# Performance work log

Measured on AMD Instinct MI355X. Metric: run time of the kernel, lower is better.

Reference implementation:

```python
import jax, jax.numpy as jnp
import numpy as np

D = 256   # input / vocab dim (hardcoded in module)
H = 256   # hidden_dim
B, M, N = 64, 32, 32
LN_EPS = 1e-6


def setup_inputs() -> dict:
    key = jax.random.key(0)
    ks = jax.random.split(key, 8)
    Hin = D + 2 * H  # column_stack([x_bd, h_i_jm1, h_im1_j])
    inp = {
        "x": jax.random.normal(ks[0], (B, M, N, D), dtype=jnp.float32),
        "W_gate": jax.random.normal(ks[1], (Hin, 5 * H), dtype=jnp.float32) * (1.0 / np.sqrt(Hin)),
        "b_gate": jnp.zeros((5 * H,), dtype=jnp.float32),
        "ln_scale": jnp.ones((H,), dtype=jnp.float32),
        "ln_bias": jnp.zeros((H,), dtype=jnp.float32),
        "W_head": jax.random.normal(ks[2], (H, D), dtype=jnp.float32) * (1.0 / np.sqrt(H)),
        "b_head": jnp.zeros((D,), dtype=jnp.float32),
        "h_init": jax.random.normal(ks[3], (H, 1), dtype=jnp.float32) * 0.05,
    }
    return inp


def _layernorm(x, scale, bias):
    mu = jnp.mean(x, axis=-1, keepdims=True)
    var = jnp.mean(jnp.square(x - mu), axis=-1, keepdims=True)
    return (x - mu) * jax.lax.rsqrt(var + LN_EPS) * scale + bias


def reference(x, W_gate, b_gate, ln_scale, ln_bias, W_head, b_head, h_init):
    b, m, n, d = x.shape
    h = h_init.shape[0]
    h0_bh = jnp.broadcast_to(h_init[:, 0][None, :], (b, h))  # left-edge init per row
    c0_bh = jnp.zeros((b, h), dtype=x.dtype)

    def col_step(carry, xs):
        h_l, c_l = carry                 # left neighbor (b,h)
        x_bd, h_u, c_u = xs              # input pixel, up-neighbor h/c
        xin = jnp.concatenate([x_bd, h_l, h_u], axis=-1)   # (b, d+2h)
        g = xin @ W_gate + b_gate                           # (b, 5h)
        f_c, f_r, i_g, o_g, g_g = jnp.split(g, 5, axis=-1)
        cell = (jax.nn.sigmoid(f_c) * c_l
                + jax.nn.sigmoid(f_r) * c_u
                + jax.nn.sigmoid(i_g) * jnp.tanh(g_g))      # (b,h)
        h_new = jax.nn.sigmoid(o_g) * jnp.tanh(_layernorm(cell, ln_scale, ln_bias))
        logits = h_new @ W_head + b_head                    # (b,d)
        return (h_new, cell), (h_new, cell, logits)

    def row_step(prev_row, x_row):
        prev_h, prev_c = prev_row        # (n,b,h) from row above
        _, (hs, cs, logits) = jax.lax.scan(col_step, (h0_bh, c0_bh), (x_row, prev_h, prev_c))
        return (hs, cs), logits          # logits: (n,b,d)

    x_mnbd = jnp.transpose(x, (1, 2, 0, 3))                 # (m,n,b,d)
    prev_h0 = jnp.broadcast_to(h_init[:, 0][None, None, :], (n, b, h)).astype(x.dtype)
    prev_c0 = jnp.zeros((n, b, h), dtype=x.dtype)
    _, logits_mnbd = jax.lax.scan(row_step, (prev_h0, prev_c0), x_mnbd)
    return jnp.transpose(logits_mnbd, (2, 0, 1, 3))         # (b,m,n,d)
```

## Files before the change

### kernel.cpp

```cpp
#include <hip/hip_runtime.h>

constexpr int kB   = 64;
constexpr int kM   = 32;
constexpr int kN   = 32;
constexpr int kD   = 256;
constexpr int kH   = 256;
constexpr int kG5  = 1280;

typedef __attribute__((ext_vector_type(8)))  short bf16x8;
typedef __attribute__((ext_vector_type(16))) float f32x16;

__device__ __forceinline__ float bu2f(unsigned short u) {
    return __uint_as_float(((unsigned)u) << 16);
}
__device__ __forceinline__ unsigned short f2bu(float f) {
    unsigned u = __float_as_uint(f);
    return (unsigned short)((u + 0x7FFF + ((u >> 16) & 1)) >> 16);
}
__device__ __forceinline__ void split1(float a, unsigned short& hi, unsigned short& lo) {
    hi = f2bu(a);
    lo = f2bu(a - bu2f(hi));
}
__device__ __forceinline__ float sigm(float x) { return 1.f / (1.f + expf(-x)); }

__global__ void prep_w(const float* __restrict__ Wg,
                       unsigned short* __restrict__ whi,
                       unsigned short* __restrict__ wlo) {
    const int t = blockIdx.x * 256 + threadIdx.x;
    const int lane = t & 63;
    const int rest = t >> 6;
    const int s = rest % 48;
    const int ntile = rest / 48;
    const int n = ntile * 32 + (lane & 31);
    const int kb = s * 16 + (lane >> 5) * 8;
    unsigned short h8[8], l8[8];
    #pragma unroll
    for (int j = 0; j < 8; ++j) {
        const float a = Wg[(size_t)(kb + j) * kG5 + n];
        split1(a, h8[j], l8[j]);
    }
    *(bf16x8*)(whi + (size_t)t * 8) = *(const bf16x8*)h8;
    *(bf16x8*)(wlo + (size_t)t * 8) = *(const bf16x8*)l8;
}

__global__ void prep_wh(const float* __restrict__ Wh,
                        unsigned short* __restrict__ whh,
                        unsigned short* __restrict__ whl) {
    const int t = blockIdx.x * 256 + threadIdx.x;
    const int lane = t & 63;
    const int rest = t >> 6;
    const int kc = rest & 15;
    const int nt = rest >> 4;
    const int n = nt * 32 + (lane & 31);
    const int kb = kc * 16 + (lane >> 5) * 8;
    unsigned short h8[8], l8[8];
    #pragma unroll
    for (int j = 0; j < 8; ++j) {
        const float a = Wh[(size_t)(kb + j) * kD + n];
        split1(a, h8[j], l8[j]);
    }
    *(bf16x8*)(whh + (size_t)t * 8) = *(const bf16x8*)h8;
    *(bf16x8*)(whl + (size_t)t * 8) = *(const bf16x8*)l8;
}

__global__ void prep_h0f(const float* __restrict__ hinit,
                         unsigned short* __restrict__ h0fh,
                         unsigned short* __restrict__ h0fl) {
    const int idx = blockIdx.x * 256 + threadIdx.x;
    const int lane = idx & 63;
    const int kh = idx >> 6;
    const int k0 = kh * 16 + (lane >> 5) * 8;
    unsigned short h8[8], l8[8];
    #pragma unroll
    for (int j = 0; j < 8; ++j) split1(hinit[k0 + j], h8[j], l8[j]);
    *(bf16x8*)(h0fh + (size_t)idx * 8) = *(const bf16x8*)h8;
    *(bf16x8*)(h0fl + (size_t)idx * 8) = *(const bf16x8*)l8;
}

__global__ void prep_x(const float* __restrict__ x,
                       unsigned short* __restrict__ xfh,
                       unsigned short* __restrict__ xfl) {
    const int t = blockIdx.x * 256 + threadIdx.x;
    const int kq   = t & 31;
    const int b    = (t >> 5) & 63;
    const int cell = t >> 11;
    const float* src = x + (((size_t)b * 1024 + cell) * kD + kq * 8);
    unsigned short h8[8], l8[8];
    #pragma unroll
    for (int j = 0; j < 8; ++j) split1(src[j], h8[j], l8[j]);
    const int mt = b >> 5, kh = kq >> 1;
    const int l  = (b & 31) + 32 * (kq & 1);
    const size_t dst = ((((size_t)cell * 2 + mt) * 16 + kh) * 64 + l) * 8;
    *(bf16x8*)(xfh + dst) = *(const bf16x8*)h8;
    *(bf16x8*)(xfl + dst) = *(const bf16x8*)l8;
}

template<bool SYNCW>
__device__ __forceinline__
void gate_body(int d, int unit,
               const unsigned short* __restrict__ xfh,
               const unsigned short* __restrict__ xfl,
               const unsigned short* __restrict__ whi,
               const unsigned short* __restrict__ wlo,
               const unsigned short* __restrict__ hfh,
               const unsigned short* __restrict__ hfl,
               const unsigned short* __restrict__ h0fh,
               const unsigned short* __restrict__ h0fl,
               float* __restrict__ gates) {
    const int tid = threadIdx.x;
    const int ilo = max(0, d - (kN - 1));
    const int cell = unit / 20;
    const int nc   = unit % 20;
    const int i = ilo + cell;
    const int j = d - i;
    const int w = tid >> 6, lane = tid & 63;
    const int ln31 = lane & 31, ln5 = lane >> 5;
    const int mt = w & 1;
    const int ntile = nc * 2 + (w >> 1);
    const int hp = (d + 1) & 1;
    const int cl = i * kN + j;

    f32x16 acc;
    #pragma unroll
    for (int r = 0; r < 16; ++r) acc[r] = 0.f;

    const unsigned short* wph = whi + ((size_t)ntile * 3072 + lane) * 8;
    const unsigned short* wpl = wlo + ((size_t)ntile * 3072 + lane) * 8;

    const unsigned short* xph = xfh + (((size_t)cl * 2 + mt) * 16 * 64 + lane) * 8;
    const unsigned short* xpl = xfl + (((size_t)cl * 2 + mt) * 16 * 64 + lane) * 8;
    #pragma unroll
    for (int kw = 0; kw < 4; ++kw) {
        if (SYNCW) __syncthreads();
        #pragma unroll
        for (int k4 = 0; k4 < 4; ++k4) {
            const int kh = kw * 4 + k4;
            const bf16x8 ah = *(const bf16x8*)(xph + (size_t)kh * 512);
            const bf16x8 al = *(const bf16x8*)(xpl + (size_t)kh * 512);
            const bf16x8 wh = *(const bf16x8*)(wph + (size_t)kh * 512);
            const bf16x8 wl = *(const bf16x8*)(wpl + (size_t)kh * 512);
            acc = __builtin_amdgcn_mfma_f32_32x32x16_bf16(ah, wh, acc, 0, 0, 0);
            acc = __builtin_amdgcn_mfma_f32_32x32x16_bf16(ah, wl, acc, 0, 0, 0);
            acc = __builtin_amdgcn_mfma_f32_32x32x16_bf16(al, wh, acc, 0, 0, 0);
        }
    }

    const unsigned short *plh, *pll, *puh, *pul;
    if (j > 0) {
        const size_t o = ((size_t)(hp * kM + i)) * 16384 + ((size_t)(mt * 16) * 64 + lane) * 8;
        plh = hfh + o; pll = hfl + o;
    } else {
        plh = h0fh + lane * 8; pll = h0fl + lane * 8;
    }
    if (i > 0) {
        const size_t o = ((size_t)(hp * kM + (i - 1))) * 16384 + ((size_t)(mt * 16) * 64 + lane) * 8;
        puh = hfh + o; pul = hfl + o;
    } else {
        puh = h0fh + lane * 8; pul = h0fl + lane * 8;
    }

    #pragma unroll
    for (int kw = 0; kw < 4; ++kw) {
        if (SYNCW) __syncthreads();
        #pragma unroll
        for (int k4 = 0; k4 < 4; ++k4) {
            const int kh = kw * 4 + k4;
            const bf16x8 ah = *(const bf16x8*)(plh + (size_t)kh * 512);
            const bf16x8 al = *(const bf16x8*)(pll + (size_t)kh * 512);
            const bf16x8 wh = *(const bf16x8*)(wph + (size_t)(16 + kh) * 512);
            const bf16x8 wl = *(const bf16x8*)(wpl + (size_t)(16 + kh) * 512);
            acc = __builtin_amdgcn_mfma_f32_32x32x16_bf16(ah, wh, acc, 0, 0, 0);
            acc = __builtin_amdgcn_mfma_f32_32x32x16_bf16(ah, wl, acc, 0, 0, 0);
            acc = __builtin_amdgcn_mfma_f32_32x32x16_bf16(al, wh, acc, 0, 0, 0);
        }
    }
    #pragma unroll
    for (int kw = 0; kw < 4; ++kw) {
        if (SYNCW) __syncthreads();
        #pragma unroll
        for (int k4 = 0; k4 < 4; ++k4) {
            const int kh = kw * 4 + k4;
            const bf16x8 ah = *(const bf16x8*)(puh + (size_t)kh * 512);
            const bf16x8 al = *(const bf16x8*)(pul + (size_t)kh * 512);
            const bf16x8 wh = *(const bf16x8*)(wph + (size_t)(32 + kh) * 512);
            const bf16x8 wl = *(const bf16x8*)(wpl + (size_t)(32 + kh) * 512);
            acc = __builtin_amdgcn_mfma_f32_32x32x16_bf16(ah, wh, acc, 0, 0, 0);
            acc = __builtin_amdgcn_mfma_f32_32x32x16_bf16(ah, wl, acc, 0, 0, 0);
            acc = __builtin_amdgcn_mfma_f32_32x32x16_bf16(al, wh, acc, 0, 0, 0);
        }
    }

    const int col = ntile * 32 + ln31;
    #pragma unroll
    for (int r = 0; r < 16; ++r) {
        const int mrow = (r & 3) + 8 * (r >> 2) + 4 * ln5;
        const int bb = mt * 32 + mrow;
        gates[((size_t)i * kB + bb) * kG5 + col] = acc[r];
    }
}

__global__ __launch_bounds__(256)
void gate_fast(int d,
               const unsigned short* __restrict__ xfh,
               const unsigned short* __restrict__ xfl,
               const unsigned short* __restrict__ whi,
               const unsigned short* __restrict__ wlo,
               const unsigned short* __restrict__ hfh,
               const unsigned short* __restrict__ hfl,
               const unsigned short* __restrict__ h0fh,
               const unsigned short* __restrict__ h0fl,
               float* __restrict__ gates) {
    gate_body<false>(d, blockIdx.x, xfh, xfl, whi, wlo, hfh, hfl, h0fh, h0fl, gates);
}

__global__ __launch_bounds__(256)
void gate_sync(int d,
               const unsigned short* __restrict__ xfh,
               const unsigned short* __restrict__ xfl,
               const unsigned short* __restrict__ whi,
               const unsigned short* __restrict__ wlo,
               const unsigned short* __restrict__ hfh,
               const unsigned short* __restrict__ hfl,
               const unsigned short* __restrict__ h0fh,
               const unsigned short* __restrict__ h0fl,
               float* __restrict__ gates) {
    gate_body<true>(d, blockIdx.x, xfh, xfl, whi, wlo, hfh, hfl, h0fh, h0fl, gates);
}

__global__ __launch_bounds__(256)
void gate_mfma_legacy(int d,
               const float* __restrict__ x,
               const unsigned short* __restrict__ whi,
               const unsigned short* __restrict__ wlo,
               const unsigned short* __restrict__ hfh,
               const unsigned short* __restrict__ hfl,
               const unsigned short* __restrict__ h0fh,
               const unsigned short* __restrict__ h0fl,
               float* __restrict__ gates) {
    const int tid = threadIdx.x;
    const int ilo = max(0, d - (kN - 1));
    const int cell = blockIdx.x / 20;
    const int nc   = blockIdx.x % 20;
    const int i = ilo + cell;
    const int j = d - i;
    const int w = tid >> 6, lane = tid & 63;
    const int ln31 = lane & 31, ln5 = lane >> 5;
    const int mt = w & 1;
    const int ntile = nc * 2 + (w >> 1);
    const int hp = (d + 1) & 1;

    f32x16 acc;
    #pragma unroll
    for (int r = 0; r < 16; ++r) acc[r] = 0.f;

    const unsigned short* wph = whi + ((size_t)ntile * 3072 + lane) * 8;
    const unsigned short* wpl = wlo + ((size_t)ntile * 3072 + lane) * 8;

    const int b = mt * 32 + ln31;
    const float* xr = x + (((size_t)b * kM + i) * kN + j) * kD + ln5 * 8;
    #pragma unroll 4
    for (int kh = 0; kh < 16; ++kh) {
        const float4 v0 = *(const float4*)(xr + kh * 16);
        const float4 v1 = *(const float4*)(xr + kh * 16 + 4);
        unsigned short h8[8], l8[8];
        split1(v0.x, h8[0], l8[0]); split1(v0.y, h8[1], l8[1]);
        split1(v0.z, h8[2], l8[2]); split1(v0.w, h8[3], l8[3]);
        split1(v1.x, h8[4], l8[4]); split1(v1.y, h8[5], l8[5]);
        split1(v1.z, h8[6], l8[6]); split1(v1.w, h8[7], l8[7]);
        const bf16x8 ah = *(const bf16x8*)h8;
        const bf16x8 al = *(const bf16x8*)l8;
        const bf16x8 wh = *(const bf16x8*)(wph + (size_t)kh * 512);
        const bf16x8 wl = *(const bf16x8*)(wpl + (size_t)kh * 512);
        acc = __builtin_amdgcn_mfma_f32_32x32x16_bf16(ah, wh, acc, 0, 0, 0);
        acc = __builtin_amdgcn_mfma_f32_32x32x16_bf16(ah, wl, acc, 0, 0, 0);
        acc = __builtin_amdgcn_mfma_f32_32x32x16_bf16(al, wh, acc, 0, 0, 0);
    }

    const unsigned short *plh, *pll, *puh, *pul;
    if (j > 0) {
        const size_t o = ((size_t)(hp * kM + i)) * 16384 + ((size_t)(mt * 16) * 64 + lane) * 8;
        plh = hfh + o; pll = hfl + o;
    } else {
        plh = h0fh + lane * 8; pll = h0fl + lane * 8;
    }
    if (i > 0) {
        const size_t o = ((size_t)(hp * kM + (i - 1))) * 16384 + ((size_t)(mt * 16) * 64 + lane) * 8;
        puh = hfh + o; pul = hfl + o;
    } else {
        puh = h0fh + lane * 8; pul = h0fl + lane * 8;
    }

    #pragma unroll 4
    for (int kh = 0; kh < 16; ++kh) {
        const bf16x8 ah = *(const bf16x8*)(plh + (size_t)kh * 512);
        const bf16x8 al = *(const bf16x8*)(pll + (size_t)kh * 512);
        const bf16x8 wh = *(const bf16x8*)(wph + (size_t)(16 + kh) * 512);
        const bf16x8 wl = *(const bf16x8*)(wpl + (size_t)(16 + kh) * 512);
        acc = __builtin_amdgcn_mfma_f32_32x32x16_bf16(ah, wh, acc, 0, 0, 0);
        acc = __builtin_amdgcn_mfma_f32_32x32x16_bf16(ah, wl, acc, 0, 0, 0);
        acc = __builtin_amdgcn_mfma_f32_32x32x16_bf16(al, wh, acc, 0, 0, 0);
    }
    #pragma unroll 4
    for (int kh = 0; kh < 16; ++kh) {
        const bf16x8 ah = *(const bf16x8*)(puh + (size_t)kh * 512);
        const bf16x8 al = *(const bf16x8*)(pul + (size_t)kh * 512);
        const bf16x8 wh = *(const bf16x8*)(wph + (size_t)(32 + kh) * 512);
        const bf16x8 wl = *(const bf16x8*)(wpl + (size_t)(32 + kh) * 512);
        acc = __builtin_amdgcn_mfma_f32_32x32x16_bf16(ah, wh, acc, 0, 0, 0);
        acc = __builtin_amdgcn_mfma_f32_32x32x16_bf16(ah, wl, acc, 0, 0, 0);
        acc = __builtin_amdgcn_mfma_f32_32x32x16_bf16(al, wh, acc, 0, 0, 0);
    }

    const int col = ntile * 32 + ln31;
    #pragma unroll
    for (int r = 0; r < 16; ++r) {
        const int mrow = (r & 3) + 8 * (r >> 2) + 4 * ln5;
        const int bb = mt * 32 + mrow;
        gates[((size_t)i * kB + bb) * kG5 + col] = acc[r];
    }
}

__global__ __launch_bounds__(256)
void cell_ln(int d,
             const float* __restrict__ bg,
             const float* __restrict__ lns,
             const float* __restrict__ lnb,
             const float* __restrict__ gates,
             float* __restrict__ c_bufs,
             unsigned short* __restrict__ hfh,
             unsigned short* __restrict__ hfl,
             float* out) {
    __shared__ float red[8];
    const int tid = threadIdx.x;
    const int ilo = max(0, d - (kN - 1));
    const int i = ilo + (blockIdx.x >> 4);
    const int j = d - i;
    const int b0 = (blockIdx.x & 15) * 4;
    const int plane = kM * kB * kH;
    const float* c_prev = c_bufs + ((d + 1) & 1) * plane;
    float*       c_cur  = c_bufs + (d & 1) * plane;
    const int hp = d & 1;
    unsigned* outp = (unsigned*)out;

    const int u = tid;
    const float bg0 = bg[u];
    const float bg1 = bg[kH + u];
    const float bg2 = bg[2 * kH + u];
    const float bg3 = bg[3 * kH + u];
    const float bg4 = bg[4 * kH + u];
    const float lnsc = lns[u];
    const float lnbi = lnb[u];
    const int lane = tid & 63, wid = tid >> 6;
    const int kh = u >> 4, r = u & 15, jj = r & 7;

    for (int bl = 0; bl < 4; ++bl) {
        const int b = b0 + bl;
        const float* grow = gates + ((size_t)i * kB + b) * kG5;
        const float fc = grow[u] + bg0;
        const float fr = grow[kH + u] + bg1;
        const float ig = grow[2 * kH + u] + bg2;
        const float og = grow[3 * kH + u] + bg3;
        const float gg = grow[4 * kH + u] + bg4;
        const float cl = (j > 0) ? c_prev[((size_t)i * kB + b) * kH + u] : 0.f;
        const float cu = (i > 0) ? c_prev[((size_t)(i - 1) * kB + b) * kH + u] : 0.f;

        const float cell_v = sigm(fc) * cl + sigm(fr) * cu + sigm(ig) * tanhf(gg);
        c_cur[((size_t)i * kB + b) * kH + u] = cell_v;

        float s = cell_v, s2 = cell_v * cell_v;
        #pragma unroll
        for (int off = 32; off; off >>= 1) {
            s  += __shfl_down(s,  off, 64);
            s2 += __shfl_down(s2, off, 64);
        }
        if (lane == 0) { red[wid] = s; red[4 + wid] = s2; }
        __syncthreads();
        const float sum = red[0] + red[1] + red[2] + red[3];
        const float sq  = red[4] + red[5] + red[6] + red[7];
        __syncthreads();

        const float mu   = sum * (1.f / kH);
        const float var  = sq * (1.f / kH) - mu * mu;
        const float rstd = rsqrtf(var + 1e-6f);
        const float hv   = sigm(og) * tanhf((cell_v - mu) * rstd * lnsc + lnbi);

        unsigned short hb, lb;
        split1(hv, hb, lb);
        const int mt2 = b >> 5;
        const int fl = (b & 31) + 32 * (r >> 3);
        const size_t fo = ((size_t)(hp * kM + i)) * 16384
                        + (((size_t)(mt2 * 16 + kh) * 64 + fl) * 8 + jj);
        hfh[fo] = hb; hfl[fo] = lb;
        outp[(((size_t)b * kM + i) * kN + j) * kD + u] = (unsigned)hb | ((unsigned)lb << 16);
    }
}

__global__ __launch_bounds__(256)
void head_mfma(const unsigned short* __restrict__ whh,
               const unsigned short* __restrict__ whl,
               const float* __restrict__ bh,
               float* out) {
    const int tid = threadIdx.x;
    const int lane = tid & 63, w = tid >> 6;
    const int ln31 = lane & 31, ln5 = lane >> 5;
    const int r0 = blockIdx.x * 64;
    const int mt = w & 1, ng = w >> 1;
    unsigned* outp = (unsigned*)out;

    f32x16 acc[4];
    #pragma unroll
    for (int t = 0; t < 4; ++t)
        #pragma unroll
        for (int r = 0; r < 16; ++r) acc[t][r] = 0.f;

    const int m = r0 + mt * 32 + ln31;
    const unsigned* arow = outp + (size_t)m * kD + ln5 * 8;

    #pragma unroll 2
    for (int kc = 0; kc < 16; ++kc) {
        const uint4 p0 = *(const uint4*)(arow + kc * 16);
        const uint4 p1 = *(const uint4*)(arow + kc * 16 + 4);
        unsigned short h8[8], l8[8];
        h8[0] = (unsigned short)(p0.x & 0xffffu); l8[0] = (unsigned short)(p0.x >> 16);
        h8[1] = (unsigned short)(p0.y & 0xffffu); l8[1] = (unsigned short)(p0.y >> 16);
        h8[2] = (unsigned short)(p0.z & 0xffffu); l8[2] = (unsigned short)(p0.z >> 16);
        h8[3] = (unsigned short)(p0.w & 0xffffu); l8[3] = (unsigned short)(p0.w >> 16);
        h8[4] = (unsigned short)(p1.x & 0xffffu); l8[4] = (unsigned short)(p1.x >> 16);
        h8[5] = (unsigned short)(p1.y & 0xffffu); l8[5] = (unsigned short)(p1.y >> 16);
        h8[6] = (unsigned short)(p1.z & 0xffffu); l8[6] = (unsigned short)(p1.z >> 16);
        h8[7] = (unsigned short)(p1.w & 0xffffu); l8[7] = (unsigned short)(p1.w >> 16);
        const bf16x8 ah = *(const bf16x8*)h8;
        const bf16x8 al = *(const bf16x8*)l8;
        #pragma unroll
        for (int t = 0; t < 4; ++t) {
            const int nt = ng * 4 + t;
            const size_t g = ((size_t)(nt * 16 + kc) * 64 + lane) * 8;
            const bf16x8 wh = *(const bf16x8*)(whh + g);
            const bf16x8 wl = *(const bf16x8*)(whl + g);
            acc[t] = __builtin_amdgcn_mfma_f32_32x32x16_bf16(ah, wh, acc[t], 0, 0, 0);
            acc[t] = __builtin_amdgcn_mfma_f32_32x32x16_bf16(ah, wl, acc[t], 0, 0, 0);
            acc[t] = __builtin_amdgcn_mfma_f32_32x32x16_bf16(al, wh, acc[t], 0, 0, 0);
        }
    }

    __syncthreads();

    #pragma unroll
    for (int t = 0; t < 4; ++t) {
        const int col = (ng * 4 + t) * 32 + ln31;
        const float bb = bh[col];
        #pragma unroll
        for (int r = 0; r < 16; ++r) {
            const int row = r0 + mt * 32 + (r & 3) + 8 * (r >> 2) + 4 * ln5;
            out[(size_t)row * kD + col] = acc[t][r] + bb;
        }
    }
}

extern "C" void kernel_launch(void* const* d_in, const int* in_sizes, int n_in,
                              void* d_out, int out_size, void* d_ws, size_t ws_size,
                              hipStream_t stream) {
    const float* x     = (const float*)d_in[0];
    const float* Wg    = (const float*)d_in[1];
    const float* bg    = (const float*)d_in[2];
    const float* lns   = (const float*)d_in[3];
    const float* lnb   = (const float*)d_in[4];
    const float* Wh    = (const float*)d_in[5];
    const float* bh    = (const float*)d_in[6];
    const float* hinit = (const float*)d_in[7];
    float* out = (float*)d_out;

    char* wsb = (char*)d_ws;
    float*          gates  = (float*)(wsb);
    float*          c_bufs = (float*)(wsb + 10485760);
    unsigned short* hfh    = (unsigned short*)(wsb + 14680064);
    unsigned short* hfl    = (unsigned short*)(wsb + 16777216);
    unsigned short* whi    = (unsigned short*)(wsb + 18874368);
    unsigned short* wlo    = (unsigned short*)(wsb + 20840448);
    unsigned short* h0fh   = (unsigned short*)(wsb + 22806528);
    unsigned short* h0fl   = (unsigned short*)(wsb + 22822912);
    unsigned short* whh    = (unsigned short*)(wsb + 22839296);
    unsigned short* whl    = (unsigned short*)(wsb + 22970368);
    unsigned short* xfh    = (unsigned short*)(wsb + 23101440);
    unsigned short* xfl    = (unsigned short*)(wsb + 56655872);
    const size_t kWsNeededFast = 90210304;

    const bool fast = (ws_size >= kWsNeededFast);

    hipLaunchKernelGGL(prep_w,  dim3(480), dim3(256), 0, stream, Wg, whi, wlo);
    hipLaunchKernelGGL(prep_wh, dim3(32),  dim3(256), 0, stream, Wh, whh, whl);
    hipLaunchKernelGGL(prep_h0f, dim3(4),  dim3(256), 0, stream, hinit, h0fh, h0fl);
    if (fast)
        hipLaunchKernelGGL(prep_x, dim3(8192), dim3(256), 0, stream, x, xfh, xfl);

    for (int d = 0; d < kM + kN - 1; ++d) {
        const int ilo = max(0, d - (kN - 1));
        const int ihi = min(d, kM - 1);
        const int ncell = ihi - ilo + 1;
        if (fast) {
            if (d & 1) {
                hipLaunchKernelGGL(gate_fast, dim3(ncell * 20), dim3(256), 0, stream,
                                   d, xfh, xfl, whi, wlo, hfh, hfl, h0fh, h0fl, gates);
            } else {
                hipLaunchKernelGGL(gate_sync, dim3(ncell * 20), dim3(256), 0, stream,
                                   d, xfh, xfl, whi, wlo, hfh, hfl, h0fh, h0fl, gates);
            }
        } else {
            hipLaunchKernelGGL(gate_mfma_legacy, dim3(ncell * 20), dim3(256), 0, stream,
                               d, x, whi, wlo, hfh, hfl, h0fh, h0fl, gates);
        }
        hipLaunchKernelGGL(cell_ln, dim3(ncell * 16), dim3(256), 0, stream,
                           d, bg, lns, lnb, gates, c_bufs, hfh, hfl, out);
    }
    hipLaunchKernelGGL(head_mfma, dim3(1024), dim3(256), 0, stream, whh, whl, bh, out);
}
```

Measured before the change: 1.621 ms.

## Add split-K gate kernel, shuffle-based cell kernel, and MFMA-ready packed h buffer

On even diagonals the gate GEMM now splits the 48 K-chunks across two wave pairs and reduces them through shared memory. This doubles the block count, which helps occupancy on the short diagonals. A new cell kernel uses one wave per batch row with shuffle reductions, replacing the block-level LN reduction on those steps. The cell kernels also write h into a separate workspace buffer already in MFMA fragment layout, and a new head kernel reads that buffer with plain vector loads instead of reshuffling. The trade-off is a larger workspace, an extra shared-memory reduction, and alternating kernel variants across diagonals.

```diff
diff --git a/kernel.cpp b/kernel.cpp
--- a/kernel.cpp
+++ b/kernel.cpp
@@ -95,9 +95,8 @@
     *(bf16x8*)(xfl + dst) = *(const bf16x8*)l8;
 }
 
-template<bool SYNCW>
-__device__ __forceinline__
-void gate_body(int d, int unit,
+__global__ __launch_bounds__(256)
+void gate_sync(int d,
                const unsigned short* __restrict__ xfh,
                const unsigned short* __restrict__ xfl,
                const unsigned short* __restrict__ whi,
@@ -109,8 +108,8 @@
                float* __restrict__ gates) {
     const int tid = threadIdx.x;
     const int ilo = max(0, d - (kN - 1));
-    const int cell = unit / 20;
-    const int nc   = unit % 20;
+    const int cell = blockIdx.x / 20;
+    const int nc   = blockIdx.x % 20;
     const int i = ilo + cell;
     const int j = d - i;
     const int w = tid >> 6, lane = tid & 63;
@@ -131,7 +130,7 @@
     const unsigned short* xpl = xfl + (((size_t)cl * 2 + mt) * 16 * 64 + lane) * 8;
     #pragma unroll
     for (int kw = 0; kw < 4; ++kw) {
-        if (SYNCW) __syncthreads();
+        __syncthreads();
         #pragma unroll
         for (int k4 = 0; k4 < 4; ++k4) {
             const int kh = kw * 4 + k4;
@@ -161,7 +160,7 @@
 
     #pragma unroll
     for (int kw = 0; kw < 4; ++kw) {
-        if (SYNCW) __syncthreads();
+        __syncthreads();
         #pragma unroll
         for (int k4 = 0; k4 < 4; ++k4) {
             const int kh = kw * 4 + k4;
@@ -176,7 +175,7 @@
     }
     #pragma unroll
     for (int kw = 0; kw < 4; ++kw) {
-        if (SYNCW) __syncthreads();
+        __syncthreads();
         #pragma unroll
         for (int k4 = 0; k4 < 4; ++k4) {
             const int kh = kw * 4 + k4;
@@ -200,31 +199,87 @@
 }
 
 __global__ __launch_bounds__(256)
-void gate_fast(int d,
-               const unsigned short* __restrict__ xfh,
-               const unsigned short* __restrict__ xfl,
-               const unsigned short* __restrict__ whi,
-               const unsigned short* __restrict__ wlo,
-               const unsigned short* __restrict__ hfh,
-               const unsigned short* __restrict__ hfl,
-               const unsigned short* __restrict__ h0fh,
-               const unsigned short* __restrict__ h0fl,
-               float* __restrict__ gates) {
-    gate_body<false>(d, blockIdx.x, xfh, xfl, whi, wlo, hfh, hfl, h0fh, h0fl, gates);
-}
-
-__global__ __launch_bounds__(256)
-void gate_sync(int d,
-               const unsigned short* __restrict__ xfh,
-               const unsigned short* __restrict__ xfl,
-               const unsigned short* __restrict__ whi,
-               const unsigned short* __restrict__ wlo,
-               const unsigned short* __restrict__ hfh,
-               const unsigned short* __restrict__ hfl,
-               const unsigned short* __restrict__ h0fh,
-               const unsigned short* __restrict__ h0fl,
-               float* __restrict__ gates) {
-    gate_body<true>(d, blockIdx.x, xfh, xfl, whi, wlo, hfh, hfl, h0fh, h0fl, gates);
+void gate_ks(int d,
+             const unsigned short* __restrict__ xfh,
+             const unsigned short* __restrict__ xfl,
+             const unsigned short* __restrict__ whi,
+             const unsigned short* __restrict__ wlo,
+             const unsigned short* __restrict__ hfh,
+             const unsigned short* __restrict__ hfl,
+             const unsigned short* __restrict__ h0fh,
+             const unsigned short* __restrict__ h0fl,
+             float* __restrict__ gates) {
+    __shared__ float accs[2][64][16];
+    const int tid = threadIdx.x;
+    const int ilo = max(0, d - (kN - 1));
+    const int cell  = blockIdx.x / 40;
+    const int ntile = blockIdx.x % 40;
+    const int i = ilo + cell;
+    const int j = d - i;
+    const int w = tid >> 6, lane = tid & 63;
+    const int ln31 = lane & 31, ln5 = lane >> 5;
+    const int mt = w & 1, ks = w >> 1;
+    const int hp = (d + 1) & 1;
+    const int cl = i * kN + j;
+
+    f32x16 acc;
+    #pragma unroll
+    for (int r = 0; r < 16; ++r) acc[r] = 0.f;
+
+    const unsigned short* wph = whi + ((size_t)ntile * 3072 + lane) * 8;
+    const unsigned short* wpl = wlo + ((size_t)ntile * 3072 + lane) * 8;
+    const unsigned short* xph = xfh + (((size_t)cl * 2 + mt) * 16 * 64 + lane) * 8;
+    const unsigned short* xpl = xfl + (((size_t)cl * 2 + mt) * 16 * 64 + lane) * 8;
+
+    const unsigned short *plh, *pll, *puh, *pul;
+    if (j > 0) {
+        const size_t o = ((size_t)(hp * kM + i)) * 16384 + ((size_t)(mt * 16) * 64 + lane) * 8;
+        plh = hfh + o; pll = hfl + o;
+    } else {
+        plh = h0fh + lane * 8; pll = h0fl + lane * 8;
+    }
+    if (i > 0) {
+        const size_t o = ((size_t)(hp * kM + (i - 1))) * 16384 + ((size_t)(mt * 16) * 64 + lane) * 8;
+        puh = hfh + o; pul = hfl + o;
+    } else {
+        puh = h0fh + lane * 8; pul = h0fl + lane * 8;
+    }
+
+    const int c0 = ks * 24;
+    for (int wdw = 0; wdw < 6; ++wdw) {
+        __syncthreads();
+        #pragma unroll
+        for (int k4 = 0; k4 < 4; ++k4) {
+            const int c = c0 + wdw * 4 + k4;
+            const unsigned short *ah_p, *al_p;
+            int co;
+            if (c < 16)      { ah_p = xph; al_p = xpl; co = c; }
+            else if (c < 32) { ah_p = plh; al_p = pll; co = c - 16; }
+            else             { ah_p = puh; al_p = pul; co = c - 32; }
+            const bf16x8 ah = *(const bf16x8*)(ah_p + (size_t)co * 512);
+            const bf16x8 al = *(const bf16x8*)(al_p + (size_t)co * 512);
+            const bf16x8 wh = *(const bf16x8*)(wph + (size_t)c * 512);
+            const bf16x8 wl = *(const bf16x8*)(wpl + (size_t)c * 512);
+            acc = __builtin_amdgcn_mfma_f32_32x32x16_bf16(ah, wh, acc, 0, 0, 0);
+            acc = __builtin_amdgcn_mfma_f32_32x32x16_bf16(ah, wl, acc, 0, 0, 0);
+            acc = __builtin_amdgcn_mfma_f32_32x32x16_bf16(al, wh, acc, 0, 0, 0);
+        }
+    }
+
+    if (ks == 1) {
+        #pragma unroll
+        for (int r = 0; r < 16; ++r) accs[mt][lane][r] = acc[r];
+    }
+    __syncthreads();
+    if (ks == 0) {
+        const int col = ntile * 32 + ln31;
+        #pragma unroll
+        for (int r = 0; r < 16; ++r) {
+            const int mrow = (r & 3) + 8 * (r >> 2) + 4 * ln5;
+            const int bb = mt * 32 + mrow;
+            gates[((size_t)i * kB + bb) * kG5 + col] = acc[r] + accs[mt][lane][r];
+        }
+    }
 }
 
 __global__ __launch_bounds__(256)
@@ -329,6 +384,7 @@
              float* __restrict__ c_bufs,
              unsigned short* __restrict__ hfh,
              unsigned short* __restrict__ hfl,
+             unsigned* __restrict__ hpk,
              float* out) {
     __shared__ float red[8];
     const int tid = threadIdx.x;
@@ -391,15 +447,102 @@
         const size_t fo = ((size_t)(hp * kM + i)) * 16384
                         + (((size_t)(mt2 * 16 + kh) * 64 + fl) * 8 + jj);
         hfh[fo] = hb; hfl[fo] = lb;
-        outp[(((size_t)b * kM + i) * kN + j) * kD + u] = (unsigned)hb | ((unsigned)lb << 16);
+        const unsigned pk = (unsigned)hb | ((unsigned)lb << 16);
+        const size_t R = ((size_t)b * kM + i) * kN + j;
+        if (hpk) {
+            const int t32 = (int)(R >> 5);
+            const int lp = ((int)R & 31) + 32 * ((u >> 3) & 1);
+            hpk[(((size_t)t32 * 16 + kh) * 64 + lp) * 8 + jj] = pk;
+        } else {
+            outp[R * kD + u] = pk;
+        }
     }
 }
 
 __global__ __launch_bounds__(256)
-void head_mfma(const unsigned short* __restrict__ whh,
-               const unsigned short* __restrict__ whl,
-               const float* __restrict__ bh,
+void cell_fast(int d,
+               const float* __restrict__ bg,
+               const float* __restrict__ lns,
+               const float* __restrict__ lnb,
+               const float* __restrict__ gates,
+               float* __restrict__ c_bufs,
+               unsigned short* __restrict__ hfh,
+               unsigned short* __restrict__ hfl,
+               unsigned* __restrict__ hpk,
                float* out) {
+    const int tid = threadIdx.x;
+    const int ilo = max(0, d - (kN - 1));
+    const int i = ilo + (blockIdx.x >> 4);
+    const int j = d - i;
+    const int b = (blockIdx.x & 15) * 4 + (tid >> 6);
+    const int q = tid & 63;
+    const int plane = kM * kB * kH;
+    const float* c_prev = c_bufs + ((d + 1) & 1) * plane;
+    float*       c_cur  = c_bufs + (d & 1) * plane;
+    const int hp = d & 1;
+    unsigned* outp = (unsigned*)out;
+
+    const float* grow = gates + ((size_t)i * kB + b) * kG5;
+    const size_t cro = ((size_t)i * kB + b) * kH;
+    const size_t cuo = ((size_t)(i - 1) * kB + b) * kH;
+
+    float cellv[4], ogv[4];
+    float s = 0.f, s2 = 0.f;
+    #pragma unroll
+    for (int k = 0; k < 4; ++k) {
+        const int u = q + 64 * k;
+        const float fc = grow[u] + bg[u];
+        const float fr = grow[kH + u] + bg[kH + u];
+        const float ig = grow[2 * kH + u] + bg[2 * kH + u];
+        const float og = grow[3 * kH + u] + bg[3 * kH + u];
+        const float gg = grow[4 * kH + u] + bg[4 * kH + u];
+        const float cl = (j > 0) ? c_prev[cro + u] : 0.f;
+        const float cu = (i > 0) ? c_prev[cuo + u] : 0.f;
+        const float cv = sigm(fc) * cl + sigm(fr) * cu + sigm(ig) * tanhf(gg);
+        c_cur[cro + u] = cv;
+        cellv[k] = cv; ogv[k] = og;
+        s += cv; s2 += cv * cv;
+    }
+    #pragma unroll
+    for (int off = 32; off; off >>= 1) {
+        s  += __shfl_down(s,  off, 64);
+        s2 += __shfl_down(s2, off, 64);
+    }
+    s  = __shfl(s, 0, 64);
+    s2 = __shfl(s2, 0, 64);
+    const float mu   = s * (1.f / kH);
+    const float var  = s2 * (1.f / kH) - mu * mu;
+    const float rstd = rsqrtf(var + 1e-6f);
+
+    const size_t R = ((size_t)b * kM + i) * kN + j;
+    const int mt2 = b >> 5;
+    #pragma unroll
+    for (int k = 0; k < 4; ++k) {
+        const int u = q + 64 * k;
+        const float hv = sigm(ogv[k]) * tanhf((cellv[k] - mu) * rstd * lns[u] + lnb[u]);
+        unsigned short hb, lb;
+        split1(hv, hb, lb);
+        const int kh = u >> 4, r = u & 15, jj = r & 7;
+        const int fl = (b & 31) + 32 * (r >> 3);
+        const size_t fo = ((size_t)(hp * kM + i)) * 16384
+                        + (((size_t)(mt2 * 16 + kh) * 64 + fl) * 8 + jj);
+        hfh[fo] = hb; hfl[fo] = lb;
+        const unsigned pk = (unsigned)hb | ((unsigned)lb << 16);
+        if (hpk) {
+            const int t32 = (int)(R >> 5);
+            const int lp = ((int)R & 31) + 32 * ((u >> 3) & 1);
+            hpk[(((size_t)t32 * 16 + kh) * 64 + lp) * 8 + jj] = pk;
+        } else {
+            outp[R * kD + u] = pk;
+        }
+    }
+}
+
+__global__ __launch_bounds__(256)
+void head_mfma64(const unsigned short* __restrict__ whh,
+                 const unsigned short* __restrict__ whl,
+                 const float* __restrict__ bh,
+                 float* out) {
     const int tid = threadIdx.x;
     const int lane = tid & 63, w = tid >> 6;
     const int ln31 = lane & 31, ln5 = lane >> 5;
@@ -457,6 +600,66 @@
     }
 }
 
+__global__ __launch_bounds__(256)
+void head_hpk(const unsigned short* __restrict__ whh,
+              const unsigned short* __restrict__ whl,
+              const float* __restrict__ bh,
+              const unsigned* __restrict__ hpk,
+              float* __restrict__ out) {
+    const int tid = threadIdx.x;
+    const int lane = tid & 63, w = tid >> 6;
+    const int ln31 = lane & 31, ln5 = lane >> 5;
+    const int r0 = blockIdx.x * 64;
+    const int mt = w & 1, ng = w >> 1;
+    const int t32 = blockIdx.x * 2 + mt;
+
+    f32x16 acc[4];
+    #pragma unroll
+    for (int t = 0; t < 4; ++t)
+        #pragma unroll
+        for (int r = 0; r < 16; ++r) acc[t][r] = 0.f;
+
+    const unsigned* ap = hpk + ((size_t)t32 * 16 * 64 + lane) * 8;
+
+    #pragma unroll 2
+    for (int kc = 0; kc < 16; ++kc) {
+        const uint4 p0 = *(const uint4*)(ap + (size_t)kc * 512);
+        const uint4 p1 = *(const uint4*)(ap + (size_t)kc * 512 + 4);
+        unsigned short h8[8], l8[8];
+        h8[0] = (unsigned short)(p0.x & 0xffffu); l8[0] = (unsigned short)(p0.x >> 16);
+        h8[1] = (unsigned short)(p0.y & 0xffffu); l8[1] = (unsigned short)(p0.y >> 16);
+        h8[2] = (unsigned short)(p0.z & 0xffffu); l8[2] = (unsigned short)(p0.z >> 16);
+        h8[3] = (unsigned short)(p0.w & 0xffffu); l8[3] = (unsigned short)(p0.w >> 16);
+        h8[4] = (unsigned short)(p1.x & 0xffffu); l8[4] = (unsigned short)(p1.x >> 16);
+        h8[5] = (unsigned short)(p1.y & 0xffffu); l8[5] = (unsigned short)(p1.y >> 16);
+        h8[6] = (unsigned short)(p1.z & 0xffffu); l8[6] = (unsigned short)(p1.z >> 16);
+        h8[7] = (unsigned short)(p1.w & 0xffffu); l8[7] = (unsigned short)(p1.w >> 16);
+        const bf16x8 ah = *(const bf16x8*)h8;
+        const bf16x8 al = *(const bf16x8*)l8;
+        #pragma unroll
+        for (int t = 0; t < 4; ++t) {
+            const int nt = ng * 4 + t;
+            const size_t g = ((size_t)(nt * 16 + kc) * 64 + lane) * 8;
+            const bf16x8 wh = *(const bf16x8*)(whh + g);
+            const bf16x8 wl = *(const bf16x8*)(whl + g);
+            acc[t] = __builtin_amdgcn_mfma_f32_32x32x16_bf16(ah, wh, acc[t], 0, 0, 0);
+            acc[t] = __builtin_amdgcn_mfma_f32_32x32x16_bf16(ah, wl, acc[t], 0, 0, 0);
+            acc[t] = __builtin_amdgcn_mfma_f32_32x32x16_bf16(al, wh, acc[t], 0, 0, 0);
+        }
+    }
+
+    #pragma unroll
+    for (int t = 0; t < 4; ++t) {
+        const int col = (ng * 4 + t) * 32 + ln31;
+        const float bb = bh[col];
+        #pragma unroll
+        for (int r = 0; r < 16; ++r) {
+            const int row = r0 + mt * 32 + (r & 3) + 8 * (r >> 2) + 4 * ln5;
+            out[(size_t)row * kD + col] = acc[t][r] + bb;
+        }
+    }
+}
+
 extern "C" void kernel_launch(void* const* d_in, const int* in_sizes, int n_in,
                               void* d_out, int out_size, void* d_ws, size_t ws_size,
                               hipStream_t stream) {
@@ -483,9 +686,13 @@
     unsigned short* whl    = (unsigned short*)(wsb + 22970368);
     unsigned short* xfh    = (unsigned short*)(wsb + 23101440);
     unsigned short* xfl    = (unsigned short*)(wsb + 56655872);
-    const size_t kWsNeededFast = 90210304;
-
-    const bool fast = (ws_size >= kWsNeededFast);
+    unsigned*       hpk    = (unsigned*)(wsb + 90210304);
+    const size_t kWsFast = 90210304;
+    const size_t kWsFull = 157319168;
+
+    const bool fast    = (ws_size >= kWsFast);
+    const bool use_hpk = (ws_size >= kWsFull);
+    unsigned* hpk_arg  = use_hpk ? hpk : (unsigned*)nullptr;
 
     hipLaunchKernelGGL(prep_w,  dim3(480), dim3(256), 0, stream, Wg, whi, wlo);
     hipLaunchKernelGGL(prep_wh, dim3(32),  dim3(256), 0, stream, Wh, whh, whl);
@@ -498,8 +705,8 @@
         const int ihi = min(d, kM - 1);
         const int ncell = ihi - ilo + 1;
         if (fast) {
-            if (d & 1) {
-                hipLaunchKernelGGL(gate_fast, dim3(ncell * 20), dim3(256), 0, stream,
+            if ((d & 1) == 0) {
+                hipLaunchKernelGGL(gate_ks, dim3(ncell * 40), dim3(256), 0, stream,
                                    d, xfh, xfl, whi, wlo, hfh, hfl, h0fh, h0fl, gates);
             } else {
                 hipLaunchKernelGGL(gate_sync, dim3(ncell * 20), dim3(256), 0, stream,
@@ -509,8 +716,17 @@
             hipLaunchKernelGGL(gate_mfma_legacy, dim3(ncell * 20), dim3(256), 0, stream,
                                d, x, whi, wlo, hfh, hfl, h0fh, h0fl, gates);
         }
-        hipLaunchKernelGGL(cell_ln, dim3(ncell * 16), dim3(256), 0, stream,
-                           d, bg, lns, lnb, gates, c_bufs, hfh, hfl, out);
-    }
-    hipLaunchKernelGGL(head_mfma, dim3(1024), dim3(256), 0, stream, whh, whl, bh, out);
-}
+        if (fast && ((d & 1) == 0)) {
+            hipLaunchKernelGGL(cell_fast, dim3(ncell * 16), dim3(256), 0, stream,
+                               d, bg, lns, lnb, gates, c_bufs, hfh, hfl, hpk_arg, out);
+        } else {
+            hipLaunchKernelGGL(cell_ln, dim3(ncell * 16), dim3(256), 0, stream,
+                               d, bg, lns, lnb, gates, c_bufs, hfh, hfl, hpk_arg, out);
+        }
+    }
+    if (use_hpk) {
+        hipLaunchKernelGGL(head_hpk, dim3(1024), dim3(256), 0, stream, whh, whl, bh, hpk, out);
+    } else {
+        hipLaunchKernelGGL(head_mfma64, dim3(1024), dim3(256), 0, stream, whh, whl, bh, out);
+    }
+}
```

New measurement: 1.554 ms. 1.04x faster.
